# Kernel tuning notes

Measured on AMD Instinct MI355X. Metric: run time of the kernel, lower is better.

The kernel has to match this reference:

```python
import jax, jax.numpy as jnp
import numpy as np

IN_SZ = 256
OUT_SZ = 256
N_CHAN = 1024
RANK = 4  # min(4, IN_SZ*OUT_SZ)
B = 256
N = 2048


def setup_inputs() -> dict:
    key = jax.random.key(0)
    k_x, k_idx, k_u, k_v, k_b = jax.random.split(key, 5)
    x = jax.random.normal(k_x, (B, N, IN_SZ), dtype=jnp.float32)
    indices = jax.random.randint(k_idx, (B,), 0, N_CHAN)
    # init per reset_parameters(const=1.0)
    bound_u = np.sqrt(3.0 / RANK)              # fan_out of weights_U [C, r] is r
    weights_U = jax.random.uniform(k_u, (N_CHAN, RANK), jnp.float32, -bound_u, bound_u)
    bound_v = np.sqrt(1.0 / (IN_SZ * OUT_SZ))  # fan_out of weights_V [r, in*out]
    weights_V = jax.random.uniform(k_v, (RANK, IN_SZ * OUT_SZ), jnp.float32, -bound_v, bound_v)
    bound_b = np.sqrt(1.0 / RANK)
    bias = jax.random.uniform(k_b, (N_CHAN, 1, OUT_SZ), jnp.float32, -bound_b, bound_b)
    return {"x": x, "indices": indices, "weights_U": weights_U,
            "weights_V": weights_V, "bias": bias}


def reference(x, indices, weights_U, weights_V, bias):
    # weight synthesis: gather U rows first, then low-rank expand (same math as
    # full (U@V)[indices], without materializing unused channels)
    w = (weights_U[indices] @ weights_V).reshape(-1, IN_SZ, OUT_SZ)  # [B, in, out]
    out = jnp.einsum('bni,bio->bno', x, w)                            # [B, N, out]
    out = out + bias[indices]                                         # [B,1,out] broadcast
    return out
```

## Files before the change

### kernel.cpp

```cpp
#include <hip/hip_runtime.h>
#include <cstdint>

typedef __attribute__((ext_vector_type(8))) short short8;
typedef __attribute__((ext_vector_type(4))) float f32x4;

constexpr int SEQ   = 2048;
constexpr int INSZ  = 256;
constexpr int OUTSZ = 256;

__device__ __forceinline__ ushort f2bf(float f) {
  union { float f; uint32_t u; } v; v.f = f;
  uint32_t u = v.u;
  return (ushort)((u + 0x7FFFu + ((u >> 16) & 1u)) >> 16);
}
__device__ __forceinline__ uint32_t pk2(float a, float b) {
  return (uint32_t)f2bf(a) | ((uint32_t)f2bf(b) << 16);
}

__global__ __launch_bounds__(256) void synth_w(
    const float* __restrict__ U, const float* __restrict__ V,
    const int* __restrict__ idx, ushort* __restrict__ wsW)
{
  const int b   = blockIdx.y;
  const int kb  = blockIdx.x;
  const int tid = threadIdx.x;
  const int ch  = idx[b];
  const float u0 = U[ch*4+0], u1 = U[ch*4+1], u2 = U[ch*4+2], u3 = U[ch*4+3];

  __shared__ ushort tile[64][260];

  const int o4    = (tid & 63) * 4;
  const int kbase = (tid >> 6) * 16;
  for (int kk = 0; kk < 16; ++kk) {
    const int k  = kbase + kk;
    const int gk = kb*64 + k;
    const float* vp = V + (size_t)gk*OUTSZ + o4;
    float4 a = *(const float4*)(vp);
    float4 c = *(const float4*)(vp + 65536);
    float4 d = *(const float4*)(vp + 131072);
    float4 e = *(const float4*)(vp + 196608);
    ushort4 pkv;
    pkv.x = f2bf(u0*a.x + u1*c.x + u2*d.x + u3*e.x);
    pkv.y = f2bf(u0*a.y + u1*c.y + u2*d.y + u3*e.y);
    pkv.z = f2bf(u0*a.z + u1*c.z + u2*d.z + u3*e.z);
    pkv.w = f2bf(u0*a.w + u1*c.w + u2*d.w + u3*e.w);
    *(ushort4*)(&tile[k][o4]) = pkv;
  }
  __syncthreads();

  for (int s = 0; s < 8; ++s) {
    const int c      = s*256 + tid;
    const int kshalf = c >> 10;
    const int nb     = (c >> 6) & 15;
    const int lane   = c & 63;
    const int o      = nb*16 + (lane & 15);
    const int k0     = kshalf*32 + (lane >> 4)*8;
    uint4 pkv;
    pkv.x = (uint32_t)tile[k0+0][o] | ((uint32_t)tile[k0+1][o] << 16);
    pkv.y = (uint32_t)tile[k0+2][o] | ((uint32_t)tile[k0+3][o] << 16);
    pkv.z = (uint32_t)tile[k0+4][o] | ((uint32_t)tile[k0+5][o] << 16);
    pkv.w = (uint32_t)tile[k0+6][o] | ((uint32_t)tile[k0+7][o] << 16);
    uint4* dst = (uint4*)(wsW + (size_t)b*65536 + (size_t)(2*kb + kshalf)*8192
                              + nb*512 + lane*8);
    *dst = pkv;
  }
}

union SmemT {
  ushort a[64*256];
  float  e[32*260];
};

__global__ __launch_bounds__(256, 4) void lr_gemm(
    const float* __restrict__ x, const int* __restrict__ idx,
    const float* __restrict__ bias, const ushort* __restrict__ wsW,
    float* __restrict__ out)
{
  __shared__ SmemT sm;

  const int wg  = blockIdx.x;
  const int swz = (wg & 7) * 1024 + (wg >> 3);
  const int b   = swz >> 5;
  const int n0  = (swz & 31) * 64;

  const int tid  = threadIdx.x;
  const int lane = tid & 63;
  const int wave = tid >> 6;
  const int hi16 = lane >> 4;
  const int lo16 = lane & 15;

  const float*  xb  = x + ((size_t)b*SEQ + n0)*INSZ;
  const ushort* wbp = wsW + (size_t)b*65536 + wave*2048 + lane*8;

  short8 bcur[4], bnxt[4];
  #pragma unroll
  for (int n = 0; n < 4; ++n)
    bcur[n] = *(const short8*)(wbp + n*512);

  #pragma unroll
  for (int it = 0; it < 8; ++it) {
    const int row = it*8 + (tid >> 5);
    const int c8  = tid & 31;
    const float* src = xb + (size_t)row*INSZ + c8*8;
    float4 f0 = *(const float4*)(src);
    float4 f1 = *(const float4*)(src + 4);
    uint4 pkv;
    pkv.x = pk2(f0.x, f0.y); pkv.y = pk2(f0.z, f0.w);
    pkv.z = pk2(f1.x, f1.y); pkv.w = pk2(f1.z, f1.w);
    *(uint4*)((char*)sm.a + row*512 + ((c8*16) ^ ((row & 7) << 4))) = pkv;
  }
  __syncthreads();

  f32x4 acc[4][4] = {};
  const int sx = (lo16 & 7) << 4;
  const char* aB = (const char*)sm.a + lo16*512;

  #pragma unroll
  for (int k5 = 0; k5 < 8; ++k5) {
    if (k5 < 7) {
      #pragma unroll
      for (int n = 0; n < 4; ++n)
        bnxt[n] = *(const short8*)(wbp + (size_t)(k5+1)*8192 + n*512);
    }
    short8 af[4];
    #pragma unroll
    for (int m = 0; m < 4; ++m)
      af[m] = *(const short8*)(aB + m*8192 + ((k5*64 + hi16*16) ^ sx));
    #pragma unroll
    for (int m = 0; m < 4; ++m)
      #pragma unroll
      for (int n = 0; n < 4; ++n)
        acc[m][n] = __builtin_amdgcn_mfma_f32_16x16x32_bf16(af[m], bcur[n], acc[m][n], 0, 0, 0);
    #pragma unroll
    for (int n = 0; n < 4; ++n) bcur[n] = bnxt[n];
  }

  const int ch = idx[b];
  const float* bb = bias + (size_t)ch*OUTSZ;
  float bv[4];
  #pragma unroll
  for (int n = 0; n < 4; ++n) bv[n] = bb[wave*64 + n*16 + lo16];

  float* outb = out + ((size_t)b*SEQ + n0)*OUTSZ;
  #pragma unroll
  for (int p = 0; p < 2; ++p) {
    __syncthreads();
    #pragma unroll
    for (int mm = 0; mm < 2; ++mm) {
      const int m = p*2 + mm;
      const int r = mm*16 + hi16*4;
      #pragma unroll
      for (int n = 0; n < 4; ++n) {
        const int col = wave*64 + n*16 + lo16;
        #pragma unroll
        for (int j = 0; j < 4; ++j)
          sm.e[(r + j)*260 + col] = acc[m][n][j] + bv[n];
      }
    }
    __syncthreads();
    #pragma unroll
    for (int q = 0; q < 8; ++q) {
      const int rl = wave*8 + q;
      float4 v = *(const float4*)&sm.e[rl*260 + lane*4];
      *(float4*)(outb + (size_t)(p*32 + rl)*OUTSZ + lane*4) = v;
    }
  }
}

extern "C" void kernel_launch(void* const* d_in, const int* in_sizes, int n_in,
                              void* d_out, int out_size, void* d_ws, size_t ws_size,
                              hipStream_t stream) {
  const float* x    = (const float*)d_in[0];
  const int*   idx  = (const int*)d_in[1];
  const float* U    = (const float*)d_in[2];
  const float* V    = (const float*)d_in[3];
  const float* bias = (const float*)d_in[4];
  float* out  = (float*)d_out;
  ushort* wsW = (ushort*)d_ws;

  synth_w<<<dim3(4, 256), 256, 0, stream>>>(U, V, idx, wsW);
  lr_gemm<<<8192, 256, 0, stream>>>(x, idx, bias, wsW, out);
}
```

Measured before the change: 248.3 us.

## Split GEMM into two row halves and write outputs directly from registers

The x tile is now processed as two 32-row halves held in separate LDS buffers. The second half's global loads are issued up front and stored to LDS during the first half's MFMA loop. The epilogue drops the LDS transpose staging and writes each accumulator element straight to global memory, which removes barriers but turns the stores into scattered 4-byte writes instead of coalesced float4 rows. The B fragments are reloaded from global for the second half, so weight traffic per block doubles.

```diff
diff --git a/kernel.cpp b/kernel.cpp
--- a/kernel.cpp
+++ b/kernel.cpp
@@ -66,17 +66,12 @@
   }
 }
 
-union SmemT {
-  ushort a[64*256];
-  float  e[32*260];
-};
-
 __global__ __launch_bounds__(256, 4) void lr_gemm(
     const float* __restrict__ x, const int* __restrict__ idx,
     const float* __restrict__ bias, const ushort* __restrict__ wsW,
     float* __restrict__ out)
 {
-  __shared__ SmemT sm;
+  __shared__ ushort ldsA[2][32*256];
 
   const int wg  = blockIdx.x;
   const int swz = (wg & 7) * 1024 + (wg >> 3);
@@ -92,48 +87,74 @@
   const float*  xb  = x + ((size_t)b*SEQ + n0)*INSZ;
   const ushort* wbp = wsW + (size_t)b*65536 + wave*2048 + lane*8;
 
+  const int row = tid >> 5;
+  const int c8  = tid & 31;
+
+  float4 s0[4][2], s1[4][2];
+  #pragma unroll
+  for (int it = 0; it < 4; ++it) {
+    const float* p = xb + (size_t)(it*8 + row)*INSZ + c8*8;
+    s0[it][0] = *(const float4*)p;
+    s0[it][1] = *(const float4*)(p + 4);
+  }
+  #pragma unroll
+  for (int it = 0; it < 4; ++it) {
+    const float* p = xb + (size_t)(32 + it*8 + row)*INSZ + c8*8;
+    s1[it][0] = *(const float4*)p;
+    s1[it][1] = *(const float4*)(p + 4);
+  }
   short8 bcur[4], bnxt[4];
   #pragma unroll
   for (int n = 0; n < 4; ++n)
     bcur[n] = *(const short8*)(wbp + n*512);
 
-  #pragma unroll
-  for (int it = 0; it < 8; ++it) {
-    const int row = it*8 + (tid >> 5);
-    const int c8  = tid & 31;
-    const float* src = xb + (size_t)row*INSZ + c8*8;
-    float4 f0 = *(const float4*)(src);
-    float4 f1 = *(const float4*)(src + 4);
+  const int wswz = ((c8*16) ^ ((row & 7) << 4));
+  #pragma unroll
+  for (int it = 0; it < 4; ++it) {
     uint4 pkv;
-    pkv.x = pk2(f0.x, f0.y); pkv.y = pk2(f0.z, f0.w);
-    pkv.z = pk2(f1.x, f1.y); pkv.w = pk2(f1.z, f1.w);
-    *(uint4*)((char*)sm.a + row*512 + ((c8*16) ^ ((row & 7) << 4))) = pkv;
+    pkv.x = pk2(s0[it][0].x, s0[it][0].y); pkv.y = pk2(s0[it][0].z, s0[it][0].w);
+    pkv.z = pk2(s0[it][1].x, s0[it][1].y); pkv.w = pk2(s0[it][1].z, s0[it][1].w);
+    *(uint4*)((char*)ldsA[0] + (it*8 + row)*512 + wswz) = pkv;
+  }
+  uint4 s1p[4];
+  #pragma unroll
+  for (int it = 0; it < 4; ++it) {
+    s1p[it].x = pk2(s1[it][0].x, s1[it][0].y); s1p[it].y = pk2(s1[it][0].z, s1[it][0].w);
+    s1p[it].z = pk2(s1[it][1].x, s1[it][1].y); s1p[it].w = pk2(s1[it][1].z, s1[it][1].w);
   }
   __syncthreads();
 
-  f32x4 acc[4][4] = {};
   const int sx = (lo16 & 7) << 4;
-  const char* aB = (const char*)sm.a + lo16*512;
-
+  const char* aB0 = (const char*)ldsA[0] + lo16*512;
+  const char* aB1 = (const char*)ldsA[1] + lo16*512;
+
+  f32x4 acc[2][4] = {};
   #pragma unroll
   for (int k5 = 0; k5 < 8; ++k5) {
+    if (k5 == 0) {
+      #pragma unroll
+      for (int it = 0; it < 4; ++it)
+        *(uint4*)((char*)ldsA[1] + (it*8 + row)*512 + wswz) = s1p[it];
+    }
     if (k5 < 7) {
       #pragma unroll
       for (int n = 0; n < 4; ++n)
         bnxt[n] = *(const short8*)(wbp + (size_t)(k5+1)*8192 + n*512);
     }
-    short8 af[4];
-    #pragma unroll
-    for (int m = 0; m < 4; ++m)
-      af[m] = *(const short8*)(aB + m*8192 + ((k5*64 + hi16*16) ^ sx));
-    #pragma unroll
-    for (int m = 0; m < 4; ++m)
+    short8 af[2];
+    #pragma unroll
+    for (int m = 0; m < 2; ++m)
+      af[m] = *(const short8*)(aB0 + m*8192 + ((k5*64 + hi16*16) ^ sx));
+    #pragma unroll
+    for (int m = 0; m < 2; ++m)
       #pragma unroll
       for (int n = 0; n < 4; ++n)
         acc[m][n] = __builtin_amdgcn_mfma_f32_16x16x32_bf16(af[m], bcur[n], acc[m][n], 0, 0, 0);
     #pragma unroll
     for (int n = 0; n < 4; ++n) bcur[n] = bnxt[n];
   }
+
+  __syncthreads();
 
   const int ch = idx[b];
   const float* bb = bias + (size_t)ch*OUTSZ;
@@ -143,26 +164,50 @@
 
   float* outb = out + ((size_t)b*SEQ + n0)*OUTSZ;
   #pragma unroll
-  for (int p = 0; p < 2; ++p) {
-    __syncthreads();
-    #pragma unroll
-    for (int mm = 0; mm < 2; ++mm) {
-      const int m = p*2 + mm;
-      const int r = mm*16 + hi16*4;
-      #pragma unroll
-      for (int n = 0; n < 4; ++n) {
-        const int col = wave*64 + n*16 + lo16;
-        #pragma unroll
-        for (int j = 0; j < 4; ++j)
-          sm.e[(r + j)*260 + col] = acc[m][n][j] + bv[n];
-      }
-    }
-    __syncthreads();
-    #pragma unroll
-    for (int q = 0; q < 8; ++q) {
-      const int rl = wave*8 + q;
-      float4 v = *(const float4*)&sm.e[rl*260 + lane*4];
-      *(float4*)(outb + (size_t)(p*32 + rl)*OUTSZ + lane*4) = v;
+  for (int m = 0; m < 2; ++m) {
+    const int r = m*16 + hi16*4;
+    #pragma unroll
+    for (int n = 0; n < 4; ++n) {
+      const int col = wave*64 + n*16 + lo16;
+      #pragma unroll
+      for (int j = 0; j < 4; ++j)
+        outb[(size_t)(r + j)*OUTSZ + col] = acc[m][n][j] + bv[n];
+    }
+  }
+
+  f32x4 acc1[2][4] = {};
+  #pragma unroll
+  for (int n = 0; n < 4; ++n)
+    bcur[n] = *(const short8*)(wbp + n*512);
+  #pragma unroll
+  for (int k5 = 0; k5 < 8; ++k5) {
+    if (k5 < 7) {
+      #pragma unroll
+      for (int n = 0; n < 4; ++n)
+        bnxt[n] = *(const short8*)(wbp + (size_t)(k5+1)*8192 + n*512);
+    }
+    short8 af[2];
+    #pragma unroll
+    for (int m = 0; m < 2; ++m)
+      af[m] = *(const short8*)(aB1 + m*8192 + ((k5*64 + hi16*16) ^ sx));
+    #pragma unroll
+    for (int m = 0; m < 2; ++m)
+      #pragma unroll
+      for (int n = 0; n < 4; ++n)
+        acc1[m][n] = __builtin_amdgcn_mfma_f32_16x16x32_bf16(af[m], bcur[n], acc1[m][n], 0, 0, 0);
+    #pragma unroll
+    for (int n = 0; n < 4; ++n) bcur[n] = bnxt[n];
+  }
+
+  #pragma unroll
+  for (int m = 0; m < 2; ++m) {
+    const int r = 32 + m*16 + hi16*4;
+    #pragma unroll
+    for (int n = 0; n < 4; ++n) {
+      const int col = wave*64 + n*16 + lo16;
+      #pragma unroll
+      for (int j = 0; j < 4; ++j)
+        outb[(size_t)(r + j)*OUTSZ + col] = acc1[m][n][j] + bv[n];
     }
   }
 }
```

After: 306.3 us. 23.4% more time.
